# Performance work log

Hardware: AMD Instinct MI355X
Metric: run time of the kernel (lower is better)

The kernel has to match this reference:

```python
import jax, jax.numpy as jnp
import numpy as np

N_NODES = 100000
N_EDGES = 1600000
IN_FEATS = 128
OUT_FEATS = 128


def setup_inputs() -> dict:
    key = jax.random.key(0)
    k1, k2, k3, k4, k5, k6, k7 = jax.random.split(key, 7)
    feat = jax.random.normal(k1, (N_NODES, IN_FEATS), dtype=jnp.float32)
    # positive per-node norms (sqrt-degree-like), shifted away from zero
    in_norm = jax.random.uniform(k2, (N_NODES,), dtype=jnp.float32) + 0.5
    out_norm = jax.random.uniform(k3, (N_NODES,), dtype=jnp.float32) + 0.5
    src = jax.random.randint(k4, (N_EDGES,), 0, N_NODES, dtype=jnp.int32)
    dst = jax.random.randint(k5, (N_EDGES,), 0, N_NODES, dtype=jnp.int32)
    # linear params, uniform(-stdv, stdv) as in reset_parameters
    stdv = 1.0 / np.sqrt(IN_FEATS)
    W = jax.random.uniform(k6, (OUT_FEATS, IN_FEATS), dtype=jnp.float32, minval=-stdv, maxval=stdv)
    b = jax.random.uniform(k7, (OUT_FEATS,), dtype=jnp.float32, minval=-stdv, maxval=stdv)
    return {"feat": feat, "in_norm": in_norm, "out_norm": out_norm,
            "src": src, "dst": dst, "W": W, "b": b}


def reference(feat, in_norm, out_norm, src, dst, W, b):
    # h_u = feat / out_norm  (per source node)
    h = feat / out_norm[:, None]                      # [N, F]
    # copy_u + sum: scatter-add source features into destination nodes
    msgs = h[src]                                     # [E, F] gather
    agg = jax.ops.segment_sum(msgs, dst, num_segments=N_NODES)  # [N, F]
    # normalize by in_norm, then linear
    out = (agg / in_norm[:, None]) @ W.T + b          # [N, F_out]
    return out
```

## Files before the change

### kernel.cpp

```cpp
#include <hip/hip_runtime.h>

#define N_NODES 100000
#define N_EDGES 1600000
#define F 128
#define NB2 391
#define BSZ 256
#define CHUNK 4000
#define CAPB 4544
#define NGROUP 6250
#define FRONT_NSORT 400
#define FRONT_NBLK 1182

#define WS_V11 32710912

typedef __attribute__((ext_vector_type(8))) short short8;
typedef __attribute__((ext_vector_type(4))) float f32x4;

__device__ __forceinline__ unsigned short f2bf(float f) {
    unsigned u = __float_as_uint(f);
    return (unsigned short)((u + 0x7fffu + ((u >> 16) & 1u)) >> 16);
}

struct SortSmem {
    int   tmpv[CHUNK];
    short tmpb[CHUNK];
    int   sorted[CHUNK];
    int   cnt[NB2];
    int   off[NB2];
    int   cur[NB2];
    int   gb[NB2];
    int   wsum[8];
};
union FrontSmem {
    short    Wb[F * F];
    SortSmem sp;
};

__global__ __launch_bounds__(512) void front_kernel(
    const float* __restrict__ feat, const float* __restrict__ out_norm,
    const int* __restrict__ src, const int* __restrict__ dst,
    const float* __restrict__ W,
    unsigned short* __restrict__ g, int* __restrict__ pool,
    int* __restrict__ gcur)
{
    __shared__ FrontSmem u;
    const int t = threadIdx.x;
    const int lane = t & 63, wv = t >> 6;

    if (blockIdx.x < FRONT_NSORT) {
        SortSmem& S = u.sp;
        for (int i = t; i < NB2; i += 512) S.cnt[i] = 0;
        __syncthreads();
        const int e0 = blockIdx.x * CHUNK;
        for (int i = t; i < CHUNK; i += 512) {
            int d = dst[e0 + i];
            int s = src[e0 + i];
            int b = d >> 8;
            S.tmpv[i] = ((d & 255) << 17) | s;
            S.tmpb[i] = (short)b;
            atomicAdd(&S.cnt[b], 1);
        }
        __syncthreads();
        int v = (t < NB2) ? S.cnt[t] : 0;
        int incl = v;
        #pragma unroll
        for (int o = 1; o < 64; o <<= 1) {
            int n = __shfl_up(incl, o);
            if (lane >= o) incl += n;
        }
        if (lane == 63) S.wsum[wv] = incl;
        __syncthreads();
        if (t < 64) {
            int vv = (t < 8) ? S.wsum[t] : 0;
            int ii = vv;
            #pragma unroll
            for (int o = 1; o < 8; o <<= 1) {
                int n = __shfl_up(ii, o);
                if (lane >= o) ii += n;
            }
            if (t < 8) S.wsum[t] = ii - vv;
        }
        __syncthreads();
        if (t < NB2) {
            int excl = incl - v + S.wsum[wv];
            S.off[t] = excl;
            S.cur[t] = excl;
        }
        __syncthreads();
        for (int j = t; j < NB2; j += 512) {
            int c = S.cnt[j];
            S.gb[j] = (c > 0) ? atomicAdd(&gcur[j], c) : 0;
        }
        __syncthreads();
        for (int i = t; i < CHUNK; i += 512) {
            int b = S.tmpb[i];
            int p = atomicAdd(&S.cur[b], 1);
            S.sorted[p] = S.tmpv[i];
        }
        __syncthreads();
        for (int j = wv; j < NB2; j += 8) {
            int c = S.cnt[j];
            if (c == 0) continue;
            int base = S.gb[j];
            int avail = CAPB - base; if (avail < 0) avail = 0;
            int lim = (c < avail) ? c : avail;
            int o = S.off[j];
            int* dp = pool + j * CAPB + base;
            for (int k = lane; k < lim; k += 64) dp[k] = S.sorted[o + k];
        }
    } else {
        #pragma unroll
        for (int i = 0; i < 4; ++i) {
            int cc = t + i * 512;
            int n = cc >> 4, kc = cc & 15;
            const float4* wp = (const float4*)(W + n * F + kc * 8);
            float4 w0 = wp[0], w1 = wp[1];
            short8 vv;
            vv[0] = (short)f2bf(w0.x); vv[1] = (short)f2bf(w0.y);
            vv[2] = (short)f2bf(w0.z); vv[3] = (short)f2bf(w0.w);
            vv[4] = (short)f2bf(w1.x); vv[5] = (short)f2bf(w1.y);
            vv[6] = (short)f2bf(w1.z); vv[7] = (short)f2bf(w1.w);
            *(short8*)&u.Wb[n * F + ((kc ^ (n & 15)) * 8)] = vv;
        }
        __syncthreads();

        const int wblk = (blockIdx.x - FRONT_NSORT) * 8 + wv;
        if (wblk >= NGROUP) return;
        const int r0 = wblk * 16;
        const int m = lane & 15, q = lane >> 4;
        const float* arow = feat + (size_t)(r0 + m) * F;
        const float rscale = 1.0f / out_norm[r0 + m];

        short8 afrag[4];
        #pragma unroll
        for (int s = 0; s < 4; ++s) {
            int k0 = s * 32 + q * 8;
            float4 x0 = *(const float4*)(arow + k0);
            float4 x1 = *(const float4*)(arow + k0 + 4);
            short8 a;
            a[0] = (short)f2bf(x0.x * rscale); a[1] = (short)f2bf(x0.y * rscale);
            a[2] = (short)f2bf(x0.z * rscale); a[3] = (short)f2bf(x0.w * rscale);
            a[4] = (short)f2bf(x1.x * rscale); a[5] = (short)f2bf(x1.y * rscale);
            a[6] = (short)f2bf(x1.z * rscale); a[7] = (short)f2bf(x1.w * rscale);
            afrag[s] = a;
        }

        f32x4 acc[8];
        #pragma unroll
        for (int cc = 0; cc < 8; ++cc) { f32x4 z = {0.f, 0.f, 0.f, 0.f}; acc[cc] = z; }

        #pragma unroll
        for (int s = 0; s < 4; ++s) {
            const int kc = s * 4 + q;
            #pragma unroll
            for (int cc = 0; cc < 8; ++cc) {
                const int n = cc * 16 + m;
                short8 wfrag = *(const short8*)&u.Wb[n * F + ((kc ^ m) * 8)];
                acc[cc] = __builtin_amdgcn_mfma_f32_16x16x32_bf16(
                    wfrag, afrag[s], acc[cc], 0, 0, 0);
            }
        }

        #pragma unroll
        for (int cc = 0; cc < 8; ++cc) {
            ushort4 o;
            o.x = f2bf(acc[cc][0]); o.y = f2bf(acc[cc][1]);
            o.z = f2bf(acc[cc][2]); o.w = f2bf(acc[cc][3]);
            *(ushort4*)&g[(size_t)(r0 + m) * F + cc * 16 + q * 4] = o;
        }
    }
}

__global__ __launch_bounds__(1024) void fsort_gather_kernel(
    const int* __restrict__ pool, const int* __restrict__ gcur,
    const unsigned short* __restrict__ g, const float* __restrict__ in_norm,
    const float* __restrict__ bias, float* __restrict__ out)
{
    __shared__ int pairs[CAPB];
    __shared__ int sorted_s[CAPB];
    __shared__ int fcnt[BSZ];
    __shared__ int s0[BSZ];
    __shared__ int sexcl[BSZ];
    __shared__ int wsum[4];
    __shared__ int woff[4];

    const int t = threadIdx.x, b = blockIdx.x;
    const int lane = t & 63, wv = t >> 6;

    if (t < BSZ) fcnt[t] = 0;
    int cnt = gcur[b];
    if (cnt > CAPB) cnt = CAPB;
    const int beg = b * CAPB;
    __syncthreads();

    for (int i = t; i < cnt; i += 1024) pairs[i] = pool[beg + i];
    __syncthreads();
    for (int i = t; i < cnt; i += 1024) atomicAdd(&fcnt[pairs[i] >> 17], 1);
    __syncthreads();

    if (t < BSZ) {
        int v = fcnt[t];
        int incl = v;
        #pragma unroll
        for (int off = 1; off < 64; off <<= 1) {
            int n = __shfl_up(incl, off);
            if (lane >= off) incl += n;
        }
        s0[t] = incl;
        if (lane == 63) wsum[wv] = incl;
    }
    __syncthreads();
    if (t < 64) {
        int v = (t < 4) ? wsum[t] : 0;
        int incl = v;
        #pragma unroll
        for (int off = 1; off < 4; off <<= 1) {
            int n = __shfl_up(incl, off);
            if (lane >= off) incl += n;
        }
        if (t < 4) woff[t] = incl - v;
    }
    __syncthreads();
    if (t < BSZ) {
        int sv = s0[t] + woff[t >> 6];
        s0[t] = sv;
        sexcl[t] = sv - fcnt[t];
    }
    __syncthreads();

    for (int i = t; i < cnt; i += 1024) {
        int p = pairs[i];
        int pos = atomicAdd(&sexcl[p >> 17], 1);
        sorted_s[pos] = p & 0x1FFFF;
    }
    __syncthreads();

    const unsigned* gp = (const unsigned*)g;
    const float2 bl = ((const float2*)bias)[lane];
    const int node0 = b << 8;
    const int nEnd = wv * 16 + 16;
    for (int nl = wv * 16; nl < nEnd; ++nl) {
        const int node = node0 + nl;
        if (node >= N_NODES) break;
        const int start = (nl == 0) ? 0 : s0[nl - 1];
        const int end = s0[nl];
        float ax = 0.f, ay = 0.f;
        int e = start;
        for (; e + 7 < end; e += 8) {
            unsigned u0 = gp[(size_t)sorted_s[e]     * 64 + lane];
            unsigned u1 = gp[(size_t)sorted_s[e + 1] * 64 + lane];
            unsigned u2 = gp[(size_t)sorted_s[e + 2] * 64 + lane];
            unsigned u3 = gp[(size_t)sorted_s[e + 3] * 64 + lane];
            unsigned u4 = gp[(size_t)sorted_s[e + 4] * 64 + lane];
            unsigned u5 = gp[(size_t)sorted_s[e + 5] * 64 + lane];
            unsigned u6 = gp[(size_t)sorted_s[e + 6] * 64 + lane];
            unsigned u7 = gp[(size_t)sorted_s[e + 7] * 64 + lane];
            ax += __uint_as_float(u0 << 16) + __uint_as_float(u1 << 16)
                + __uint_as_float(u2 << 16) + __uint_as_float(u3 << 16)
                + __uint_as_float(u4 << 16) + __uint_as_float(u5 << 16)
                + __uint_as_float(u6 << 16) + __uint_as_float(u7 << 16);
            ay += __uint_as_float(u0 & 0xffff0000u) + __uint_as_float(u1 & 0xffff0000u)
                + __uint_as_float(u2 & 0xffff0000u) + __uint_as_float(u3 & 0xffff0000u)
                + __uint_as_float(u4 & 0xffff0000u) + __uint_as_float(u5 & 0xffff0000u)
                + __uint_as_float(u6 & 0xffff0000u) + __uint_as_float(u7 & 0xffff0000u);
        }
        for (; e + 3 < end; e += 4) {
            unsigned u0 = gp[(size_t)sorted_s[e]     * 64 + lane];
            unsigned u1 = gp[(size_t)sorted_s[e + 1] * 64 + lane];
            unsigned u2 = gp[(size_t)sorted_s[e + 2] * 64 + lane];
            unsigned u3 = gp[(size_t)sorted_s[e + 3] * 64 + lane];
            ax += __uint_as_float(u0 << 16) + __uint_as_float(u1 << 16)
                + __uint_as_float(u2 << 16) + __uint_as_float(u3 << 16);
            ay += __uint_as_float(u0 & 0xffff0000u) + __uint_as_float(u1 & 0xffff0000u)
                + __uint_as_float(u2 & 0xffff0000u) + __uint_as_float(u3 & 0xffff0000u);
        }
        for (; e < end; ++e) {
            unsigned u = gp[(size_t)sorted_s[e] * 64 + lane];
            ax += __uint_as_float(u << 16);
            ay += __uint_as_float(u & 0xffff0000u);
        }
        const float rin = 1.0f / in_norm[node];
        float2 o; o.x = ax * rin + bl.x; o.y = ay * rin + bl.y;
        ((float2*)out)[(size_t)node * 64 + lane] = o;
    }
}

__global__ __launch_bounds__(256) void scatter_kernel(
    const float* __restrict__ feat, const float* __restrict__ out_norm,
    const int* __restrict__ src, const int* __restrict__ dst,
    float* __restrict__ agg)
{
    const int wave = threadIdx.x >> 6;
    const int lane = threadIdx.x & 63;
    const int e = blockIdx.x * 4 + wave;
    const int s = src[e];
    const int d = dst[e];
    const float rn = 1.0f / out_norm[s];
    const float2 v = ((const float2*)(feat + (size_t)s * F))[lane];
    float* ap = agg + (size_t)d * F + lane * 2;
    unsafeAtomicAdd(ap,     v.x * rn);
    unsafeAtomicAdd(ap + 1, v.y * rn);
}

__global__ __launch_bounds__(256) void transform_kernel(
    float* __restrict__ out, const float* __restrict__ in_norm,
    const float* __restrict__ W, const float* __restrict__ bias)
{
    __shared__ float Wt[F * F];
    const int t = threadIdx.x;
    #pragma unroll
    for (int i = 0; i < (F * F) / 256; ++i) {
        int idx = t + i * 256;
        int j = idx >> 7;
        int k = idx & (F - 1);
        Wt[k * F + j] = W[idx];
    }
    __syncthreads();
    const int wave = t >> 6, lane = t & 63;
    const float b0 = bias[lane];
    const float b1 = bias[lane + 64];
    const int ngroups = N_NODES / 16;
    for (int gi = blockIdx.x; gi < ngroups; gi += gridDim.x) {
        const int r = gi * 16 + wave * 4;
        const float4* a0 = (const float4*)(out + (size_t)r * F);
        const float4* a1 = a0 + F / 4;
        const float4* a2 = a0 + 2 * (F / 4);
        const float4* a3 = a0 + 3 * (F / 4);
        float acc00 = 0.f, acc01 = 0.f, acc10 = 0.f, acc11 = 0.f;
        float acc20 = 0.f, acc21 = 0.f, acc30 = 0.f, acc31 = 0.f;
        for (int k4 = 0; k4 < F / 4; ++k4) {
            const float4 x0 = a0[k4]; const float4 x1 = a1[k4];
            const float4 x2 = a2[k4]; const float4 x3 = a3[k4];
            const float xs0[4] = {x0.x, x0.y, x0.z, x0.w};
            const float xs1[4] = {x1.x, x1.y, x1.z, x1.w};
            const float xs2[4] = {x2.x, x2.y, x2.z, x2.w};
            const float xs3[4] = {x3.x, x3.y, x3.z, x3.w};
            #pragma unroll
            for (int kk = 0; kk < 4; ++kk) {
                const int k = k4 * 4 + kk;
                const float w0 = Wt[k * F + lane];
                const float w1 = Wt[k * F + 64 + lane];
                acc00 = fmaf(xs0[kk], w0, acc00); acc01 = fmaf(xs0[kk], w1, acc01);
                acc10 = fmaf(xs1[kk], w0, acc10); acc11 = fmaf(xs1[kk], w1, acc11);
                acc20 = fmaf(xs2[kk], w0, acc20); acc21 = fmaf(xs2[kk], w1, acc21);
                acc30 = fmaf(xs3[kk], w0, acc30); acc31 = fmaf(xs3[kk], w1, acc31);
            }
        }
        const float i0 = 1.0f / in_norm[r + 0];
        const float i1 = 1.0f / in_norm[r + 1];
        const float i2 = 1.0f / in_norm[r + 2];
        const float i3 = 1.0f / in_norm[r + 3];
        out[(size_t)(r + 0) * F + lane]      = acc00 * i0 + b0;
        out[(size_t)(r + 0) * F + 64 + lane] = acc01 * i0 + b1;
        out[(size_t)(r + 1) * F + lane]      = acc10 * i1 + b0;
        out[(size_t)(r + 1) * F + 64 + lane] = acc11 * i1 + b1;
        out[(size_t)(r + 2) * F + lane]      = acc20 * i2 + b0;
        out[(size_t)(r + 2) * F + 64 + lane] = acc21 * i2 + b1;
        out[(size_t)(r + 3) * F + lane]      = acc30 * i3 + b0;
        out[(size_t)(r + 3) * F + 64 + lane] = acc31 * i3 + b1;
    }
}

extern "C" void kernel_launch(void* const* d_in, const int* in_sizes, int n_in,
                              void* d_out, int out_size, void* d_ws, size_t ws_size,
                              hipStream_t stream) {
    const float* feat     = (const float*)d_in[0];
    const float* in_norm  = (const float*)d_in[1];
    const float* out_norm = (const float*)d_in[2];
    const int*   src      = (const int*)d_in[3];
    const int*   dst      = (const int*)d_in[4];
    const float* W        = (const float*)d_in[5];
    const float* b        = (const float*)d_in[6];
    float* out = (float*)d_out;

    if (ws_size >= (size_t)WS_V11) {
        char* w = (char*)d_ws;
        int*            pool = (int*)(w + 0);
        int*            gcur = (int*)(w + 7106816);
        unsigned short* g    = (unsigned short*)(w + 7110912);

        hipMemsetAsync(gcur, 0, 4096, stream);
        front_kernel<<<FRONT_NBLK, 512, 0, stream>>>(
            feat, out_norm, src, dst, W, g, pool, gcur);
        fsort_gather_kernel<<<NB2, 1024, 0, stream>>>(
            pool, gcur, g, in_norm, b, out);
    } else {
        hipMemsetAsync(out, 0, (size_t)N_NODES * F * sizeof(float), stream);
        scatter_kernel<<<N_EDGES / 4, 256, 0, stream>>>(feat, out_norm, src, dst, out);
        transform_kernel<<<2048, 256, 0, stream>>>(out, in_norm, W, b);
    }
}
```

Measured before the change: 198.4 us.

## Fuse front and gather phases into one cooperative kernel with grid syncs

Replaces the memset plus two-kernel pipeline with a single cooperative launch of 512 blocks of 1024 threads. Grid-wide syncs separate the bucket-sort/GEMM phase from the gather phase, and the sort blocks also take a share of the GEMM tiles to balance load. The aim is to remove launch and memset overhead and the tail between kernels. In exchange it needs two resident 1024-thread blocks per CU, pays for grid-sync barriers, and each block re-converts W to bf16. If the occupancy check fails, it falls back to the old path.

```diff
diff --git a/kernel.cpp b/kernel.cpp
--- a/kernel.cpp
+++ b/kernel.cpp
@@ -1,4 +1,7 @@
 #include <hip/hip_runtime.h>
+#include <hip/hip_cooperative_groups.h>
+
+namespace cg = cooperative_groups;
 
 #define N_NODES 100000
 #define N_EDGES 1600000
@@ -10,6 +13,10 @@
 #define NGROUP 6250
 #define FRONT_NSORT 400
 #define FRONT_NBLK 1182
+#define GRID_F 512
+#define NTPB 1024
+#define TILES_NS 5376
+#define TILES_SORT (NGROUP - TILES_NS)
 
 #define WS_V11 32710912
 
@@ -19,6 +26,285 @@
 __device__ __forceinline__ unsigned short f2bf(float f) {
     unsigned u = __float_as_uint(f);
     return (unsigned short)((u + 0x7fffu + ((u >> 16) & 1u)) >> 16);
+}
+
+__device__ __forceinline__ void gemm_tile16(
+    int tile, const float* __restrict__ feat, const float* __restrict__ out_norm,
+    const short* __restrict__ Wb, unsigned short* __restrict__ g, int lane)
+{
+    const int r0 = tile * 16;
+    const int m = lane & 15, q = lane >> 4;
+    const float* arow = feat + (size_t)(r0 + m) * F;
+    const float rscale = 1.0f / out_norm[r0 + m];
+
+    short8 afrag[4];
+    #pragma unroll
+    for (int s = 0; s < 4; ++s) {
+        int k0 = s * 32 + q * 8;
+        float4 x0 = *(const float4*)(arow + k0);
+        float4 x1 = *(const float4*)(arow + k0 + 4);
+        short8 a;
+        a[0] = (short)f2bf(x0.x * rscale); a[1] = (short)f2bf(x0.y * rscale);
+        a[2] = (short)f2bf(x0.z * rscale); a[3] = (short)f2bf(x0.w * rscale);
+        a[4] = (short)f2bf(x1.x * rscale); a[5] = (short)f2bf(x1.y * rscale);
+        a[6] = (short)f2bf(x1.z * rscale); a[7] = (short)f2bf(x1.w * rscale);
+        afrag[s] = a;
+    }
+
+    #pragma unroll
+    for (int half = 0; half < 2; ++half) {
+        f32x4 acc[4];
+        #pragma unroll
+        for (int c4 = 0; c4 < 4; ++c4) { f32x4 z = {0.f, 0.f, 0.f, 0.f}; acc[c4] = z; }
+        #pragma unroll
+        for (int s = 0; s < 4; ++s) {
+            const int kc = s * 4 + q;
+            #pragma unroll
+            for (int c4 = 0; c4 < 4; ++c4) {
+                const int n = (half * 4 + c4) * 16 + m;
+                short8 wfrag = *(const short8*)&Wb[n * F + ((kc ^ m) * 8)];
+                acc[c4] = __builtin_amdgcn_mfma_f32_16x16x32_bf16(
+                    wfrag, afrag[s], acc[c4], 0, 0, 0);
+            }
+        }
+        #pragma unroll
+        for (int c4 = 0; c4 < 4; ++c4) {
+            ushort4 o;
+            o.x = f2bf(acc[c4][0]); o.y = f2bf(acc[c4][1]);
+            o.z = f2bf(acc[c4][2]); o.w = f2bf(acc[c4][3]);
+            *(ushort4*)&g[(size_t)(r0 + m) * F + (half * 4 + c4) * 16 + q * 4] = o;
+        }
+    }
+}
+
+union FusedSmem {
+    struct {
+        short Wb[F * F];
+        int   tmpv[CHUNK];
+        short tmpb[CHUNK];
+        int   sorted[CHUNK];
+        int   cnt[NB2];
+        int   off[NB2];
+        int   cur[NB2];
+        int   gb[NB2];
+        int   wsum[16];
+    } p1;
+    struct {
+        int pairs[CAPB];
+        int sorted_s[CAPB];
+        int fcnt[BSZ];
+        int s0[BSZ];
+        int sexcl[BSZ];
+        int wsum[4];
+        int woff[4];
+    } p2;
+};
+
+__global__ __launch_bounds__(NTPB, 8) void fused_kernel(
+    const float* __restrict__ feat, const float* __restrict__ out_norm,
+    const int* __restrict__ src, const int* __restrict__ dst,
+    const float* __restrict__ W, const float* __restrict__ in_norm,
+    const float* __restrict__ bias,
+    unsigned short* __restrict__ g, int* __restrict__ pool,
+    int* __restrict__ gcur, float* __restrict__ out)
+{
+    __shared__ FusedSmem u;
+    cg::grid_group gg = cg::this_grid();
+    const int t = threadIdx.x, b = blockIdx.x;
+    const int lane = t & 63, wv = t >> 6;
+
+    #pragma unroll
+    for (int i = 0; i < 2; ++i) {
+        int cc = t + i * NTPB;
+        int n = cc >> 4, kc = cc & 15;
+        const float4* wp = (const float4*)(W + n * F + kc * 8);
+        float4 w0 = wp[0], w1 = wp[1];
+        short8 vv;
+        vv[0] = (short)f2bf(w0.x); vv[1] = (short)f2bf(w0.y);
+        vv[2] = (short)f2bf(w0.z); vv[3] = (short)f2bf(w0.w);
+        vv[4] = (short)f2bf(w1.x); vv[5] = (short)f2bf(w1.y);
+        vv[6] = (short)f2bf(w1.z); vv[7] = (short)f2bf(w1.w);
+        *(short8*)&u.p1.Wb[n * F + ((kc ^ (n & 15)) * 8)] = vv;
+    }
+    if (b == 0 && t < NB2) gcur[t] = 0;
+    __threadfence();
+    gg.sync();
+
+    if (b < FRONT_NSORT) {
+        auto& S = u.p1;
+        if (t < NB2) S.cnt[t] = 0;
+        __syncthreads();
+        const int e0 = b * CHUNK;
+        for (int i = t; i < CHUNK; i += NTPB) {
+            int d = dst[e0 + i];
+            int s = src[e0 + i];
+            int bb = d >> 8;
+            S.tmpv[i] = ((d & 255) << 17) | s;
+            S.tmpb[i] = (short)bb;
+            atomicAdd(&S.cnt[bb], 1);
+        }
+        __syncthreads();
+        int v = (t < NB2) ? S.cnt[t] : 0;
+        int incl = v;
+        #pragma unroll
+        for (int o = 1; o < 64; o <<= 1) {
+            int n = __shfl_up(incl, o);
+            if (lane >= o) incl += n;
+        }
+        if (lane == 63) S.wsum[wv] = incl;
+        __syncthreads();
+        if (t < 64) {
+            int vv = (t < 16) ? S.wsum[t] : 0;
+            int ii = vv;
+            #pragma unroll
+            for (int o = 1; o < 16; o <<= 1) {
+                int n = __shfl_up(ii, o);
+                if (lane >= o) ii += n;
+            }
+            if (t < 16) S.wsum[t] = ii - vv;
+        }
+        __syncthreads();
+        if (t < NB2) {
+            int excl = incl - v + S.wsum[wv];
+            S.off[t] = excl;
+            S.cur[t] = excl;
+        }
+        __syncthreads();
+        if (t < NB2) {
+            int c = S.cnt[t];
+            S.gb[t] = (c > 0) ? atomicAdd(&gcur[t], c) : 0;
+        }
+        __syncthreads();
+        for (int i = t; i < CHUNK; i += NTPB) {
+            int bb = S.tmpb[i];
+            int p = atomicAdd(&S.cur[bb], 1);
+            S.sorted[p] = S.tmpv[i];
+        }
+        __syncthreads();
+        for (int j = wv; j < NB2; j += 16) {
+            int c = S.cnt[j];
+            if (c == 0) continue;
+            int base = S.gb[j];
+            int avail = CAPB - base; if (avail < 0) avail = 0;
+            int lim = (c < avail) ? c : avail;
+            int o = S.off[j];
+            int* dp = pool + j * CAPB + base;
+            for (int k = lane; k < lim; k += 64) dp[k] = S.sorted[o + k];
+        }
+        int Wid = b * 16 + wv;
+        if (Wid < TILES_SORT) gemm_tile16(TILES_NS + Wid, feat, out_norm, u.p1.Wb, g, lane);
+    } else {
+        __syncthreads();
+        int Wn = (b - FRONT_NSORT) * 16 + wv;
+        #pragma unroll
+        for (int j = 0; j < 3; ++j) {
+            int tile = Wn * 3 + j;
+            if (tile < TILES_NS) gemm_tile16(tile, feat, out_norm, u.p1.Wb, g, lane);
+        }
+    }
+    __threadfence();
+    gg.sync();
+    __threadfence();
+
+    if (b < NB2) {
+        auto& S2 = u.p2;
+        if (t < BSZ) S2.fcnt[t] = 0;
+        int cnt = gcur[b];
+        if (cnt > CAPB) cnt = CAPB;
+        const int beg = b * CAPB;
+        __syncthreads();
+
+        for (int i = t; i < cnt; i += NTPB) S2.pairs[i] = pool[beg + i];
+        __syncthreads();
+        for (int i = t; i < cnt; i += NTPB) atomicAdd(&S2.fcnt[S2.pairs[i] >> 17], 1);
+        __syncthreads();
+
+        if (t < BSZ) {
+            int v = S2.fcnt[t];
+            int incl = v;
+            #pragma unroll
+            for (int off = 1; off < 64; off <<= 1) {
+                int n = __shfl_up(incl, off);
+                if (lane >= off) incl += n;
+            }
+            S2.s0[t] = incl;
+            if (lane == 63) S2.wsum[wv] = incl;
+        }
+        __syncthreads();
+        if (t < 64) {
+            int v = (t < 4) ? S2.wsum[t] : 0;
+            int incl = v;
+            #pragma unroll
+            for (int off = 1; off < 4; off <<= 1) {
+                int n = __shfl_up(incl, off);
+                if (lane >= off) incl += n;
+            }
+            if (t < 4) S2.woff[t] = incl - v;
+        }
+        __syncthreads();
+        if (t < BSZ) {
+            int sv = S2.s0[t] + S2.woff[t >> 6];
+            S2.s0[t] = sv;
+            S2.sexcl[t] = sv - S2.fcnt[t];
+        }
+        __syncthreads();
+
+        for (int i = t; i < cnt; i += NTPB) {
+            int p = S2.pairs[i];
+            int pos = atomicAdd(&S2.sexcl[p >> 17], 1);
+            S2.sorted_s[pos] = p & 0x1FFFF;
+        }
+        __syncthreads();
+
+        const unsigned* gp = (const unsigned*)g;
+        const float2 bl = ((const float2*)bias)[lane];
+        const int node0 = b << 8;
+        const int nEnd = wv * 16 + 16;
+        for (int nl = wv * 16; nl < nEnd; ++nl) {
+            const int node = node0 + nl;
+            if (node >= N_NODES) break;
+            const int start = (nl == 0) ? 0 : S2.s0[nl - 1];
+            const int end = S2.s0[nl];
+            float ax = 0.f, ay = 0.f;
+            int e = start;
+            for (; e + 7 < end; e += 8) {
+                unsigned u0 = gp[(size_t)S2.sorted_s[e]     * 64 + lane];
+                unsigned u1 = gp[(size_t)S2.sorted_s[e + 1] * 64 + lane];
+                unsigned u2 = gp[(size_t)S2.sorted_s[e + 2] * 64 + lane];
+                unsigned u3 = gp[(size_t)S2.sorted_s[e + 3] * 64 + lane];
+                unsigned u4 = gp[(size_t)S2.sorted_s[e + 4] * 64 + lane];
+                unsigned u5 = gp[(size_t)S2.sorted_s[e + 5] * 64 + lane];
+                unsigned u6 = gp[(size_t)S2.sorted_s[e + 6] * 64 + lane];
+                unsigned u7 = gp[(size_t)S2.sorted_s[e + 7] * 64 + lane];
+                ax += __uint_as_float(u0 << 16) + __uint_as_float(u1 << 16)
+                    + __uint_as_float(u2 << 16) + __uint_as_float(u3 << 16)
+                    + __uint_as_float(u4 << 16) + __uint_as_float(u5 << 16)
+                    + __uint_as_float(u6 << 16) + __uint_as_float(u7 << 16);
+                ay += __uint_as_float(u0 & 0xffff0000u) + __uint_as_float(u1 & 0xffff0000u)
+                    + __uint_as_float(u2 & 0xffff0000u) + __uint_as_float(u3 & 0xffff0000u)
+                    + __uint_as_float(u4 & 0xffff0000u) + __uint_as_float(u5 & 0xffff0000u)
+                    + __uint_as_float(u6 & 0xffff0000u) + __uint_as_float(u7 & 0xffff0000u);
+            }
+            for (; e + 3 < end; e += 4) {
+                unsigned u0 = gp[(size_t)S2.sorted_s[e]     * 64 + lane];
+                unsigned u1 = gp[(size_t)S2.sorted_s[e + 1] * 64 + lane];
+                unsigned u2 = gp[(size_t)S2.sorted_s[e + 2] * 64 + lane];
+                unsigned u3 = gp[(size_t)S2.sorted_s[e + 3] * 64 + lane];
+                ax += __uint_as_float(u0 << 16) + __uint_as_float(u1 << 16)
+                    + __uint_as_float(u2 << 16) + __uint_as_float(u3 << 16);
+                ay += __uint_as_float(u0 & 0xffff0000u) + __uint_as_float(u1 & 0xffff0000u)
+                    + __uint_as_float(u2 & 0xffff0000u) + __uint_as_float(u3 & 0xffff0000u);
+            }
+            for (; e < end; ++e) {
+                unsigned uu = gp[(size_t)S2.sorted_s[e] * 64 + lane];
+                ax += __uint_as_float(uu << 16);
+                ay += __uint_as_float(uu & 0xffff0000u);
+            }
+            const float rin = 1.0f / in_norm[node];
+            float2 o; o.x = ax * rin + bl.x; o.y = ay * rin + bl.y;
+            ((float2*)out)[(size_t)node * 64 + lane] = o;
+        }
+    }
 }
 
 struct SortSmem {
@@ -123,51 +409,9 @@
             *(short8*)&u.Wb[n * F + ((kc ^ (n & 15)) * 8)] = vv;
         }
         __syncthreads();
-
         const int wblk = (blockIdx.x - FRONT_NSORT) * 8 + wv;
         if (wblk >= NGROUP) return;
-        const int r0 = wblk * 16;
-        const int m = lane & 15, q = lane >> 4;
-        const float* arow = feat + (size_t)(r0 + m) * F;
-        const float rscale = 1.0f / out_norm[r0 + m];
-
-        short8 afrag[4];
-        #pragma unroll
-        for (int s = 0; s < 4; ++s) {
-            int k0 = s * 32 + q * 8;
-            float4 x0 = *(const float4*)(arow + k0);
-            float4 x1 = *(const float4*)(arow + k0 + 4);
-            short8 a;
-            a[0] = (short)f2bf(x0.x * rscale); a[1] = (short)f2bf(x0.y * rscale);
-            a[2] = (short)f2bf(x0.z * rscale); a[3] = (short)f2bf(x0.w * rscale);
-            a[4] = (short)f2bf(x1.x * rscale); a[5] = (short)f2bf(x1.y * rscale);
-            a[6] = (short)f2bf(x1.z * rscale); a[7] = (short)f2bf(x1.w * rscale);
-            afrag[s] = a;
-        }
-
-        f32x4 acc[8];
-        #pragma unroll
-        for (int cc = 0; cc < 8; ++cc) { f32x4 z = {0.f, 0.f, 0.f, 0.f}; acc[cc] = z; }
-
-        #pragma unroll
-        for (int s = 0; s < 4; ++s) {
-            const int kc = s * 4 + q;
-            #pragma unroll
-            for (int cc = 0; cc < 8; ++cc) {
-                const int n = cc * 16 + m;
-                short8 wfrag = *(const short8*)&u.Wb[n * F + ((kc ^ m) * 8)];
-                acc[cc] = __builtin_amdgcn_mfma_f32_16x16x32_bf16(
-                    wfrag, afrag[s], acc[cc], 0, 0, 0);
-            }
-        }
-
-        #pragma unroll
-        for (int cc = 0; cc < 8; ++cc) {
-            ushort4 o;
-            o.x = f2bf(acc[cc][0]); o.y = f2bf(acc[cc][1]);
-            o.z = f2bf(acc[cc][2]); o.w = f2bf(acc[cc][3]);
-            *(ushort4*)&g[(size_t)(r0 + m) * F + cc * 16 + q * 4] = o;
-        }
+        gemm_tile16(wblk, feat, out_norm, u.Wb, g, lane);
     }
 }
 
@@ -275,9 +519,9 @@
                 + __uint_as_float(u2 & 0xffff0000u) + __uint_as_float(u3 & 0xffff0000u);
         }
         for (; e < end; ++e) {
-            unsigned u = gp[(size_t)sorted_s[e] * 64 + lane];
-            ax += __uint_as_float(u << 16);
-            ay += __uint_as_float(u & 0xffff0000u);
+            unsigned uu = gp[(size_t)sorted_s[e] * 64 + lane];
+            ax += __uint_as_float(uu << 16);
+            ay += __uint_as_float(uu & 0xffff0000u);
         }
         const float rin = 1.0f / in_norm[node];
         float2 o; o.x = ax * rin + bl.x; o.y = ay * rin + bl.y;
@@ -379,11 +623,31 @@
         int*            gcur = (int*)(w + 7106816);
         unsigned short* g    = (unsigned short*)(w + 7110912);
 
-        hipMemsetAsync(gcur, 0, 4096, stream);
-        front_kernel<<<FRONT_NBLK, 512, 0, stream>>>(
-            feat, out_norm, src, dst, W, g, pool, gcur);
-        fsort_gather_kernel<<<NB2, 1024, 0, stream>>>(
-            pool, gcur, g, in_norm, b, out);
+        static int s_mode = -1;
+        if (s_mode < 0) {
+            int dev = 0;
+            hipGetDevice(&dev);
+            int coop = 0;
+            hipDeviceGetAttribute(&coop, hipDeviceAttributeCooperativeLaunch, dev);
+            int maxb = 0;
+            hipError_t oe = hipOccupancyMaxActiveBlocksPerMultiprocessor(
+                &maxb, fused_kernel, NTPB, 0);
+            s_mode = (coop != 0 && oe == hipSuccess && maxb >= 2) ? 1 : 0;
+        }
+
+        if (s_mode == 1) {
+            void* ka[] = { (void*)&feat, (void*)&out_norm, (void*)&src, (void*)&dst,
+                           (void*)&W, (void*)&in_norm, (void*)&b,
+                           (void*)&g, (void*)&pool, (void*)&gcur, (void*)&out };
+            hipLaunchCooperativeKernel(fused_kernel, dim3(GRID_F), dim3(NTPB),
+                                       ka, 0, stream);
+        } else {
+            hipMemsetAsync(gcur, 0, 4096, stream);
+            front_kernel<<<FRONT_NBLK, 512, 0, stream>>>(
+                feat, out_norm, src, dst, W, g, pool, gcur);
+            fsort_gather_kernel<<<NB2, 1024, 0, stream>>>(
+                pool, gcur, g, in_norm, b, out);
+        }
     } else {
         hipMemsetAsync(out, 0, (size_t)N_NODES * F * sizeof(float), stream);
         scatter_kernel<<<N_EDGES / 4, 256, 0, stream>>>(feat, out_norm, src, dst, out);
```

New measurement: 196.3 us. Within noise of the previous version (-1.1%).

## Replace global atomic bucket allocation with per-chunk count/offset matrices

Applied to the files above, without the earlier changes.

The sort blocks now write their locally sorted chunk contiguously to the pool and record per-bucket counts and offsets in small matrices, instead of claiming space in each bucket with global atomics. The gather kernel prefix-scans these counts per bucket and assembles its pairs from 400 chunk segments. This removes the hipMemsetAsync launch and the global atomic contention. In exchange the gather side does more fragmented reads and an extra scan. The GEMM path is also split into two halves of four accumulators to lower register pressure.

```diff
diff --git a/kernel.cpp b/kernel.cpp
--- a/kernel.cpp
+++ b/kernel.cpp
@@ -11,7 +11,7 @@
 #define FRONT_NSORT 400
 #define FRONT_NBLK 1182
 
-#define WS_V11 32710912
+#define WS_V13 32625600
 
 typedef __attribute__((ext_vector_type(8))) short short8;
 typedef __attribute__((ext_vector_type(4))) float f32x4;
@@ -19,6 +19,55 @@
 __device__ __forceinline__ unsigned short f2bf(float f) {
     unsigned u = __float_as_uint(f);
     return (unsigned short)((u + 0x7fffu + ((u >> 16) & 1u)) >> 16);
+}
+
+__device__ __forceinline__ void gemm_tile16(
+    int tile, const float* __restrict__ feat, const float* __restrict__ out_norm,
+    const short* __restrict__ Wb, unsigned short* __restrict__ g, int lane)
+{
+    const int r0 = tile * 16;
+    const int m = lane & 15, q = lane >> 4;
+    const float* arow = feat + (size_t)(r0 + m) * F;
+    const float rscale = 1.0f / out_norm[r0 + m];
+
+    short8 afrag[4];
+    #pragma unroll
+    for (int s = 0; s < 4; ++s) {
+        int k0 = s * 32 + q * 8;
+        float4 x0 = *(const float4*)(arow + k0);
+        float4 x1 = *(const float4*)(arow + k0 + 4);
+        short8 a;
+        a[0] = (short)f2bf(x0.x * rscale); a[1] = (short)f2bf(x0.y * rscale);
+        a[2] = (short)f2bf(x0.z * rscale); a[3] = (short)f2bf(x0.w * rscale);
+        a[4] = (short)f2bf(x1.x * rscale); a[5] = (short)f2bf(x1.y * rscale);
+        a[6] = (short)f2bf(x1.z * rscale); a[7] = (short)f2bf(x1.w * rscale);
+        afrag[s] = a;
+    }
+
+    #pragma unroll
+    for (int half = 0; half < 2; ++half) {
+        f32x4 acc[4];
+        #pragma unroll
+        for (int c4 = 0; c4 < 4; ++c4) { f32x4 z = {0.f, 0.f, 0.f, 0.f}; acc[c4] = z; }
+        #pragma unroll
+        for (int s = 0; s < 4; ++s) {
+            const int kc = s * 4 + q;
+            #pragma unroll
+            for (int c4 = 0; c4 < 4; ++c4) {
+                const int n = (half * 4 + c4) * 16 + m;
+                short8 wfrag = *(const short8*)&Wb[n * F + ((kc ^ m) * 8)];
+                acc[c4] = __builtin_amdgcn_mfma_f32_16x16x32_bf16(
+                    wfrag, afrag[s], acc[c4], 0, 0, 0);
+            }
+        }
+        #pragma unroll
+        for (int c4 = 0; c4 < 4; ++c4) {
+            ushort4 o;
+            o.x = f2bf(acc[c4][0]); o.y = f2bf(acc[c4][1]);
+            o.z = f2bf(acc[c4][2]); o.w = f2bf(acc[c4][3]);
+            *(ushort4*)&g[(size_t)(r0 + m) * F + (half * 4 + c4) * 16 + q * 4] = o;
+        }
+    }
 }
 
 struct SortSmem {
@@ -28,7 +77,6 @@
     int   cnt[NB2];
     int   off[NB2];
     int   cur[NB2];
-    int   gb[NB2];
     int   wsum[8];
 };
 union FrontSmem {
@@ -41,7 +89,7 @@
     const int* __restrict__ src, const int* __restrict__ dst,
     const float* __restrict__ W,
     unsigned short* __restrict__ g, int* __restrict__ pool,
-    int* __restrict__ gcur)
+    unsigned short* __restrict__ cntM, unsigned short* __restrict__ offM)
 {
     __shared__ FrontSmem u;
     const int t = threadIdx.x;
@@ -49,9 +97,10 @@
 
     if (blockIdx.x < FRONT_NSORT) {
         SortSmem& S = u.sp;
-        for (int i = t; i < NB2; i += 512) S.cnt[i] = 0;
-        __syncthreads();
-        const int e0 = blockIdx.x * CHUNK;
+        const int blk = blockIdx.x;
+        if (t < NB2) S.cnt[t] = 0;
+        __syncthreads();
+        const int e0 = blk * CHUNK;
         for (int i = t; i < CHUNK; i += 512) {
             int d = dst[e0 + i];
             int s = src[e0 + i];
@@ -87,26 +136,16 @@
             S.cur[t] = excl;
         }
         __syncthreads();
-        for (int j = t; j < NB2; j += 512) {
-            int c = S.cnt[j];
-            S.gb[j] = (c > 0) ? atomicAdd(&gcur[j], c) : 0;
-        }
-        __syncthreads();
         for (int i = t; i < CHUNK; i += 512) {
             int b = S.tmpb[i];
             int p = atomicAdd(&S.cur[b], 1);
             S.sorted[p] = S.tmpv[i];
         }
         __syncthreads();
-        for (int j = wv; j < NB2; j += 8) {
-            int c = S.cnt[j];
-            if (c == 0) continue;
-            int base = S.gb[j];
-            int avail = CAPB - base; if (avail < 0) avail = 0;
-            int lim = (c < avail) ? c : avail;
-            int o = S.off[j];
-            int* dp = pool + j * CAPB + base;
-            for (int k = lane; k < lim; k += 64) dp[k] = S.sorted[o + k];
+        for (int i = t; i < CHUNK; i += 512) pool[blk * CHUNK + i] = S.sorted[i];
+        if (t < NB2) {
+            cntM[t * FRONT_NSORT + blk] = (unsigned short)S.cnt[t];
+            offM[t * FRONT_NSORT + blk] = (unsigned short)S.off[t];
         }
     } else {
         #pragma unroll
@@ -123,102 +162,104 @@
             *(short8*)&u.Wb[n * F + ((kc ^ (n & 15)) * 8)] = vv;
         }
         __syncthreads();
-
         const int wblk = (blockIdx.x - FRONT_NSORT) * 8 + wv;
         if (wblk >= NGROUP) return;
-        const int r0 = wblk * 16;
-        const int m = lane & 15, q = lane >> 4;
-        const float* arow = feat + (size_t)(r0 + m) * F;
-        const float rscale = 1.0f / out_norm[r0 + m];
-
-        short8 afrag[4];
-        #pragma unroll
-        for (int s = 0; s < 4; ++s) {
-            int k0 = s * 32 + q * 8;
-            float4 x0 = *(const float4*)(arow + k0);
-            float4 x1 = *(const float4*)(arow + k0 + 4);
-            short8 a;
-            a[0] = (short)f2bf(x0.x * rscale); a[1] = (short)f2bf(x0.y * rscale);
-            a[2] = (short)f2bf(x0.z * rscale); a[3] = (short)f2bf(x0.w * rscale);
-            a[4] = (short)f2bf(x1.x * rscale); a[5] = (short)f2bf(x1.y * rscale);
-            a[6] = (short)f2bf(x1.z * rscale); a[7] = (short)f2bf(x1.w * rscale);
-            afrag[s] = a;
-        }
-
-        f32x4 acc[8];
-        #pragma unroll
-        for (int cc = 0; cc < 8; ++cc) { f32x4 z = {0.f, 0.f, 0.f, 0.f}; acc[cc] = z; }
-
-        #pragma unroll
-        for (int s = 0; s < 4; ++s) {
-            const int kc = s * 4 + q;
-            #pragma unroll
-            for (int cc = 0; cc < 8; ++cc) {
-                const int n = cc * 16 + m;
-                short8 wfrag = *(const short8*)&u.Wb[n * F + ((kc ^ m) * 8)];
-                acc[cc] = __builtin_amdgcn_mfma_f32_16x16x32_bf16(
-                    wfrag, afrag[s], acc[cc], 0, 0, 0);
-            }
-        }
-
-        #pragma unroll
-        for (int cc = 0; cc < 8; ++cc) {
-            ushort4 o;
-            o.x = f2bf(acc[cc][0]); o.y = f2bf(acc[cc][1]);
-            o.z = f2bf(acc[cc][2]); o.w = f2bf(acc[cc][3]);
-            *(ushort4*)&g[(size_t)(r0 + m) * F + cc * 16 + q * 4] = o;
-        }
+        gemm_tile16(wblk, feat, out_norm, u.Wb, g, lane);
     }
 }
 
 __global__ __launch_bounds__(1024) void fsort_gather_kernel(
-    const int* __restrict__ pool, const int* __restrict__ gcur,
+    const int* __restrict__ pool, const unsigned short* __restrict__ cntM,
+    const unsigned short* __restrict__ offM,
     const unsigned short* __restrict__ g, const float* __restrict__ in_norm,
     const float* __restrict__ bias, float* __restrict__ out)
 {
     __shared__ int pairs[CAPB];
     __shared__ int sorted_s[CAPB];
+    __shared__ int cntL[FRONT_NSORT];
+    __shared__ int offL[FRONT_NSORT];
+    __shared__ int runB[FRONT_NSORT];
     __shared__ int fcnt[BSZ];
     __shared__ int s0[BSZ];
     __shared__ int sexcl[BSZ];
-    __shared__ int wsum[4];
+    __shared__ int wsum[8];
     __shared__ int woff[4];
 
     const int t = threadIdx.x, b = blockIdx.x;
     const int lane = t & 63, wv = t >> 6;
 
+    if (t < FRONT_NSORT) {
+        cntL[t] = cntM[b * FRONT_NSORT + t];
+        offL[t] = offM[b * FRONT_NSORT + t];
+    }
     if (t < BSZ) fcnt[t] = 0;
-    int cnt = gcur[b];
+    __syncthreads();
+
+    int v = 0, incl = 0;
+    if (t < 512) {
+        v = (t < FRONT_NSORT) ? cntL[t] : 0;
+        incl = v;
+        #pragma unroll
+        for (int o = 1; o < 64; o <<= 1) {
+            int n = __shfl_up(incl, o);
+            if (lane >= o) incl += n;
+        }
+        if (lane == 63) wsum[wv] = incl;
+        if (t < FRONT_NSORT) runB[t] = incl - v;
+    }
+    __syncthreads();
+    if (t < 64) {
+        int vv = (t < 8) ? wsum[t] : 0;
+        int ii = vv;
+        #pragma unroll
+        for (int o = 1; o < 8; o <<= 1) {
+            int n = __shfl_up(ii, o);
+            if (lane >= o) ii += n;
+        }
+        if (t < 8) wsum[t] = ii - vv;
+    }
+    __syncthreads();
+    if (t < FRONT_NSORT) runB[t] += wsum[t >> 6];
+    __syncthreads();
+
+    for (int r = wv; r < FRONT_NSORT; r += 16) {
+        int L = cntL[r];
+        if (L <= 0) continue;
+        int base = runB[r];
+        if (base >= CAPB) continue;
+        int lim = L;
+        if (lim > CAPB - base) lim = CAPB - base;
+        const int srcb = r * CHUNK + offL[r];
+        for (int l = lane; l < lim; l += 64) pairs[base + l] = pool[srcb + l];
+    }
+    __syncthreads();
+    int cnt = runB[FRONT_NSORT - 1] + cntL[FRONT_NSORT - 1];
     if (cnt > CAPB) cnt = CAPB;
-    const int beg = b * CAPB;
-    __syncthreads();
-
-    for (int i = t; i < cnt; i += 1024) pairs[i] = pool[beg + i];
-    __syncthreads();
+
     for (int i = t; i < cnt; i += 1024) atomicAdd(&fcnt[pairs[i] >> 17], 1);
     __syncthreads();
 
     if (t < BSZ) {
-        int v = fcnt[t];
-        int incl = v;
+        int vv = fcnt[t];
+        int ii = vv;
         #pragma unroll
         for (int off = 1; off < 64; off <<= 1) {
-            int n = __shfl_up(incl, off);
-            if (lane >= off) incl += n;
-        }
-        s0[t] = incl;
-        if (lane == 63) wsum[wv] = incl;
+            int n = __shfl_up(ii, off);
+            if (lane >= off) ii += n;
+        }
+        s0[t] = ii;
+        if (lane == 63) wsum[wv] = ii;
     }
     __syncthreads();
     if (t < 64) {
-        int v = (t < 4) ? wsum[t] : 0;
-        int incl = v;
+        int vv = (t < 4) ? wsum[t] : 0;
+        int ii = vv;
         #pragma unroll
         for (int off = 1; off < 4; off <<= 1) {
-            int n = __shfl_up(incl, off);
-            if (lane >= off) incl += n;
-        }
-        if (t < 4) woff[t] = incl - v;
+            int n = __shfl_up(ii, off);
+            if (lane >= off) ii += n;
+        }
+        if (t < 4) woff[t] = ii - vv;
     }
     __syncthreads();
     if (t < BSZ) {
@@ -275,9 +316,9 @@
                 + __uint_as_float(u2 & 0xffff0000u) + __uint_as_float(u3 & 0xffff0000u);
         }
         for (; e < end; ++e) {
-            unsigned u = gp[(size_t)sorted_s[e] * 64 + lane];
-            ax += __uint_as_float(u << 16);
-            ay += __uint_as_float(u & 0xffff0000u);
+            unsigned uu = gp[(size_t)sorted_s[e] * 64 + lane];
+            ax += __uint_as_float(uu << 16);
+            ay += __uint_as_float(uu & 0xffff0000u);
         }
         const float rin = 1.0f / in_norm[node];
         float2 o; o.x = ax * rin + bl.x; o.y = ay * rin + bl.y;
@@ -373,17 +414,17 @@
     const float* b        = (const float*)d_in[6];
     float* out = (float*)d_out;
 
-    if (ws_size >= (size_t)WS_V11) {
+    if (ws_size >= (size_t)WS_V13) {
         char* w = (char*)d_ws;
         int*            pool = (int*)(w + 0);
-        int*            gcur = (int*)(w + 7106816);
-        unsigned short* g    = (unsigned short*)(w + 7110912);
-
-        hipMemsetAsync(gcur, 0, 4096, stream);
+        unsigned short* cntM = (unsigned short*)(w + 6400000);
+        unsigned short* offM = (unsigned short*)(w + 6712800);
+        unsigned short* g    = (unsigned short*)(w + 7025600);
+
         front_kernel<<<FRONT_NBLK, 512, 0, stream>>>(
-            feat, out_norm, src, dst, W, g, pool, gcur);
+            feat, out_norm, src, dst, W, g, pool, cntM, offM);
         fsort_gather_kernel<<<NB2, 1024, 0, stream>>>(
-            pool, gcur, g, in_norm, b, out);
+            pool, cntM, offM, g, in_norm, b, out);
     } else {
         hipMemsetAsync(out, 0, (size_t)N_NODES * F * sizeof(float), stream);
         scatter_kernel<<<N_EDGES / 4, 256, 0, stream>>>(feat, out_norm, src, dst, out);
```

After: 240.8 us. +21.4%, slower.
